# Optimization experiments

Measured on AMD Instinct MI355X. Metric: run time of the kernel, lower is better.

Reference implementation:

```python
import jax, jax.numpy as jnp
import numpy as np

D = 256
EXP = 4


def layer_norm(x, gamma, beta, eps=1e-5):
    mu = jnp.mean(x, axis=-1, keepdims=True)
    var = jnp.var(x, axis=-1, keepdims=True)
    return (x - mu) / jnp.sqrt(var + eps) * gamma + beta


def setup_inputs() -> dict:
    key = jax.random.key(0)
    ks = jax.random.split(key, 7)
    B, N = 8, 2048
    x = jax.random.normal(ks[0], (B, N, D), dtype=jnp.float32)
    w1 = jax.random.normal(ks[1], (D, EXP * D), dtype=jnp.float32) * (1.0 / np.sqrt(D))
    b1 = jnp.zeros((EXP * D,), dtype=jnp.float32)
    w2 = jax.random.normal(ks[2], (EXP * D, D), dtype=jnp.float32) * (1.0 / np.sqrt(EXP * D))
    b2 = jnp.zeros((D,), dtype=jnp.float32)
    g1 = jnp.ones((D,), dtype=jnp.float32)
    be1 = jnp.zeros((D,), dtype=jnp.float32)
    g2 = jnp.ones((D,), dtype=jnp.float32)
    be2 = jnp.zeros((D,), dtype=jnp.float32)
    return {"x": x, "w1": w1, "b1": b1, "w2": w2, "b2": b2,
            "gamma1": g1, "beta1": be1, "gamma2": g2, "beta2": be2}


def reference(x, w1, b1, w2, b2, gamma1, beta1, gamma2, beta2):
    # Sublayer 1: x + SA(LN(x)); SA uses raw QK^T softmax with Q=K=V=LN(x)
    h = layer_norm(x, gamma1, beta1)               # [B,N,D]
    scale = jnp.sqrt(jnp.float32(h.shape[-1]))
    scores = jnp.einsum('bnd,bmd->bnm', h, h) / scale  # [B,N,N]
    prob = jax.nn.softmax(scores, axis=-1)
    sa_out = jnp.einsum('bnm,bmd->bnd', prob, h)
    x = x + sa_out
    # Sublayer 2: x + FFN(LN(x))
    h2 = layer_norm(x, gamma2, beta2)
    ffn = jax.nn.relu(h2 @ w1 + b1) @ w2 + b2
    return x + ffn
```

## Files before the change

kernel.cpp:

```cpp
#include <hip/hip_runtime.h>
#include <hip/hip_bf16.h>

typedef unsigned short u16;
typedef unsigned int u32;
typedef __attribute__((ext_vector_type(8))) short short8;
typedef __attribute__((ext_vector_type(4))) float f32x4;

typedef unsigned int __attribute__((address_space(1))) as1_u32;
typedef unsigned int __attribute__((address_space(3))) as3_u32;

__device__ __forceinline__ void gload16(const void* g, void* l) {
    __builtin_amdgcn_global_load_lds((const as1_u32*)g, (as3_u32*)l, 16, 0, 0);
}

__device__ __forceinline__ u16 f2b(float f) {
    union { float f; unsigned u; } v; v.f = f;
    unsigned r = v.u + 0x7fffu + ((v.u >> 16) & 1u);
    return (u16)(r >> 16);
}

__global__ void transpose_cast(const float* __restrict__ src,
                               u16* __restrict__ dst, int R, int C) {
    __shared__ float tile[32][33];
    const int c0 = blockIdx.x * 32, r0 = blockIdx.y * 32;
    const int tx = threadIdx.x, ty = threadIdx.y;
#pragma unroll
    for (int i = ty; i < 32; i += 8)
        tile[i][tx] = src[(size_t)(r0 + i) * C + c0 + tx];
    __syncthreads();
#pragma unroll
    for (int i = ty; i < 32; i += 8)
        dst[(size_t)(c0 + i) * R + r0 + tx] = f2b(tile[tx][i]);
}

__global__ void transpose_bf16(const u16* __restrict__ src, u16* __restrict__ dst) {
    __shared__ u16 t[32][33];
    const int b = blockIdx.z;
    const int n0 = blockIdx.x * 32, d0 = blockIdx.y * 32;
    const int tx = threadIdx.x, ty = threadIdx.y;
    const u16* s = src + (size_t)b * (2048 * 256);
    u16* d = dst + (size_t)b * (2048 * 256);
#pragma unroll
    for (int i = ty; i < 32; i += 8)
        t[i][tx] = s[(size_t)(n0 + i) * 256 + d0 + tx];
    __syncthreads();
#pragma unroll
    for (int i = ty; i < 32; i += 8)
        d[(size_t)(d0 + i) * 2048 + n0 + tx] = t[tx][i];
}

__global__ __launch_bounds__(256) void ln_kernel(
    const float* __restrict__ x, const float* __restrict__ g,
    const float* __restrict__ be, u16* __restrict__ out) {
    const int lane = threadIdx.x & 63;
    const size_t row = (size_t)blockIdx.x * 4 + (threadIdx.x >> 6);
    const float4 v = *((const float4*)(x + row * 256) + lane);
    float s  = v.x + v.y + v.z + v.w;
    float s2 = v.x * v.x + v.y * v.y + v.z * v.z + v.w * v.w;
#pragma unroll
    for (int m = 1; m < 64; m <<= 1) {
        s  += __shfl_xor(s, m);
        s2 += __shfl_xor(s2, m);
    }
    const float mean = s * (1.0f / 256.0f);
    const float var  = s2 * (1.0f / 256.0f) - mean * mean;
    const float rstd = rsqrtf(var + 1e-5f);
    const float4 gv = *((const float4*)g + lane);
    const float4 bv = *((const float4*)be + lane);
    ushort4 o;
    o.x = f2b((v.x - mean) * rstd * gv.x + bv.x);
    o.y = f2b((v.y - mean) * rstd * gv.y + bv.y);
    o.z = f2b((v.z - mean) * rstd * gv.z + bv.z);
    o.w = f2b((v.w - mean) * rstd * gv.w + bv.w);
    *((ushort4*)(out + row * 256) + lane) = o;
}

#define ATTN_LDS_BYTES (2*65536 + 8*16*40*2)

__global__ __launch_bounds__(512) void attn_kernel(
    const u16* __restrict__ h, const u16* __restrict__ hT,
    const float* __restrict__ x, float* __restrict__ xmid) {
    extern __shared__ char smem[];
    const int tid  = threadIdx.x;
    const int w    = tid >> 6;
    const int lane = tid & 63;
    const int grp  = lane >> 4;
    const int l16  = lane & 15;
    const int qsub = w & 3;
    const int kh   = w >> 2;
    const int b    = blockIdx.y;
    const int q0   = blockIdx.x * 64;

    const u16* hb = h + (size_t)b * (2048 * 256);
    const char* hbB = (const char*)hb;
    const char* hTB = (const char*)(hT + (size_t)b * (2048 * 256));
    char* myPb = smem + 131072 + w * 1280;

    short8 qf[8];
    {
        const u16* qp = hb + (size_t)(q0 + qsub * 16 + l16) * 256 + grp * 8;
#pragma unroll
        for (int kk = 0; kk < 8; ++kk) qf[kk] = *(const short8*)(qp + kk * 32);
    }

    f32x4 oacc[16];
#pragma unroll
    for (int n = 0; n < 16; ++n) oacc[n] = (f32x4){0.f, 0.f, 0.f, 0.f};
    float m_run = -1e30f;
    float l_run = 0.f;

    const char* gK0 = hbB + ((size_t)(tid >> 5) << 9)
                          + (((tid & 31) ^ ((tid >> 5) & 7)) << 4);
    const char* gV0 = hTB + ((size_t)(tid >> 3) << 12)
                          + (((tid & 7) ^ ((tid >> 3) & 7)) << 4);

    {
        char* lK = smem + w * 1024;
        char* lV = smem + 32768 + w * 1024;
#pragma unroll
        for (int it = 0; it < 4; ++it) gload16(gK0 + (size_t)it * 8192, lK + it * 8192);
#pragma unroll
        for (int it = 0; it < 4; ++it) gload16(gV0 + (size_t)it * 262144, lV + it * 8192);
    }
    __syncthreads();

    for (int kt = 0; kt < 32; ++kt) {
        const int cur = kt & 1;
        if (kt < 31) {
            char* lK = smem + (cur ^ 1) * 65536 + w * 1024;
            char* lV = smem + (cur ^ 1) * 65536 + 32768 + w * 1024;
            const char* gK = gK0 + (size_t)(kt + 1) * 32768;
            const char* gV = gV0 + (size_t)(kt + 1) * 128;
#pragma unroll
            for (int it = 0; it < 4; ++it) gload16(gK + (size_t)it * 8192, lK + it * 8192);
#pragma unroll
            for (int it = 0; it < 4; ++it) gload16(gV + (size_t)it * 262144, lV + it * 8192);
        }
        const char* KBb = smem + cur * 65536;
        const char* VBb = KBb + 32768;

        f32x4 sacc[2];
#pragma unroll
        for (int j = 0; j < 2; ++j) sacc[j] = (f32x4){0.f, 0.f, 0.f, 0.f};
#pragma unroll
        for (int j = 0; j < 2; ++j) {
            const char* rb = KBb + ((kh * 32 + j * 16 + l16) << 9);
#pragma unroll
            for (int kk = 0; kk < 8; ++kk) {
                const int c = grp + 4 * kk;
                const int swz = (c & ~7) | ((c ^ l16) & 7);
                sacc[j] = __builtin_amdgcn_mfma_f32_16x16x32_bf16(
                    *(const short8*)(rb + (swz << 4)), qf[kk], sacc[j], 0, 0, 0);
            }
        }

        float p[2][4];
#pragma unroll
        for (int j = 0; j < 2; ++j)
#pragma unroll
            for (int r = 0; r < 4; ++r) p[j][r] = sacc[j][r] * 0.0625f;
        float m = p[0][0];
#pragma unroll
        for (int j = 0; j < 2; ++j)
#pragma unroll
            for (int r = 0; r < 4; ++r) m = fmaxf(m, p[j][r]);
        m = fmaxf(m, __shfl_xor(m, 16));
        m = fmaxf(m, __shfl_xor(m, 32));
        if (__any(m > m_run + 8.f)) {
            const float mnew  = fmaxf(m_run, m);
            const float alpha = __expf(m_run - mnew);
            m_run = mnew;
            l_run *= alpha;
            float ar[4];
#pragma unroll
            for (int r = 0; r < 4; ++r) ar[r] = __shfl(alpha, grp * 4 + r);
#pragma unroll
            for (int n = 0; n < 16; ++n)
#pragma unroll
                for (int r = 0; r < 4; ++r) oacc[n][r] *= ar[r];
        }
        float lt = 0.f;
#pragma unroll
        for (int j = 0; j < 2; ++j)
#pragma unroll
            for (int r = 0; r < 4; ++r) {
                p[j][r] = __expf(p[j][r] - m_run);
                lt += p[j][r];
            }
        lt += __shfl_xor(lt, 16);
        lt += __shfl_xor(lt, 32);
        l_run += lt;

#pragma unroll
        for (int j = 0; j < 2; ++j)
#pragma unroll
            for (int rp = 0; rp < 2; ++rp) {
                const u32 pk = (u32)f2b(p[j][rp * 2]) | ((u32)f2b(p[j][rp * 2 + 1]) << 16);
                *(u32*)(myPb + l16 * 80 + (j * 16 + grp * 4 + rp * 2) * 2) = pk;
            }

        {
            const short8 pa = *(const short8*)(myPb + l16 * 80 + grp * 16);
            const int cc2 = ((kh << 2) + grp) ^ (l16 & 7);
#pragma unroll
            for (int n = 0; n < 16; ++n) {
                const short8 bv =
                    *(const short8*)(VBb + ((n * 16 + l16) << 7) + (cc2 << 4));
                oacc[n] = __builtin_amdgcn_mfma_f32_16x16x32_bf16(pa, bv, oacc[n], 0, 0, 0);
            }
        }
        __syncthreads();
    }

    const int pair = w & 3;
    if (w >= 4) {
#pragma unroll
        for (int n = 0; n < 16; ++n)
            *(f32x4*)(smem + pair * 16384 + (n * 16 + l16) * 64 + grp * 16) = oacc[n];
        if (lane < 16) {
            float* mlp = (float*)(smem + 131072 + pair * 128);
            mlp[l16 * 2]     = m_run;
            mlp[l16 * 2 + 1] = l_run;
        }
    }
    __syncthreads();
    if (w < 4) {
        float c0[4], c1[4];
        {
            const float* mlp = (const float*)(smem + 131072 + w * 128);
#pragma unroll
            for (int r = 0; r < 4; ++r) {
                const float m0 = __shfl(m_run, grp * 4 + r);
                const float l0 = __shfl(l_run, grp * 4 + r);
                const float m1 = mlp[(grp * 4 + r) * 2];
                const float l1 = mlp[(grp * 4 + r) * 2 + 1];
                const float M  = fmaxf(m0, m1);
                const float a0 = __expf(m0 - M);
                const float a1 = __expf(m1 - M);
                const float inv = 1.0f / (l0 * a0 + l1 * a1);
                c0[r] = a0 * inv;
                c1[r] = a1 * inv;
            }
        }
        const float* xb = x + (size_t)b * (2048 * 256);
        float* ob = xmid + (size_t)b * (2048 * 256);
#pragma unroll
        for (int n = 0; n < 16; ++n) {
            const f32x4 o1 = *(const f32x4*)(smem + w * 16384 + (n * 16 + l16) * 64 + grp * 16);
#pragma unroll
            for (int r = 0; r < 4; ++r) {
                const int row = q0 + w * 16 + grp * 4 + r;
                const size_t idx = (size_t)row * 256 + n * 16 + l16;
                ob[idx] = xb[idx] + oacc[n][r] * c0[r] + o1[r] * c1[r];
            }
        }
    }
}

#define FFN_LDS_BYTES (2*65536 + 8*16*40*2 + 4096)

__global__ __launch_bounds__(512) void ffn_kernel(
    const u16* __restrict__ h2, const u16* __restrict__ w1t,
    const u16* __restrict__ w2t, const float* __restrict__ b1,
    const float* __restrict__ b2, float* __restrict__ xmid) {
    extern __shared__ char smem[];
    const int tid  = threadIdx.x;
    const int w    = tid >> 6;
    const int lane = tid & 63;
    const int grp  = lane >> 4;
    const int l16  = lane & 15;
    const int qsub = w & 3;
    const int hh   = w >> 2;
    const int t0   = blockIdx.x * 64;
    char* myAb = smem + 131072 + w * 1280;
    const char* b1lds = smem + 141312;

    short8 af[8];
    {
        const u16* ap = h2 + (size_t)(t0 + qsub * 16 + l16) * 256 + grp * 8;
#pragma unroll
        for (int kk = 0; kk < 8; ++kk) af[kk] = *(const short8*)(ap + kk * 32);
    }

    f32x4 oacc[16];
#pragma unroll
    for (int n = 0; n < 16; ++n) oacc[n] = (f32x4){0.f, 0.f, 0.f, 0.f};

    const char* g10 = (const char*)w1t + ((size_t)(tid >> 5) << 9)
                                       + (((tid & 31) ^ ((tid >> 5) & 7)) << 4);
    const char* g20 = (const char*)w2t + ((size_t)(tid >> 3) << 11)
                                       + (((tid & 7) ^ ((tid >> 3) & 7)) << 4);

    {
        char* l1 = smem + w * 1024;
        char* l2 = smem + 32768 + w * 1024;
#pragma unroll
        for (int it = 0; it < 4; ++it) gload16(g10 + (size_t)it * 8192, l1 + it * 8192);
#pragma unroll
        for (int it = 0; it < 4; ++it) gload16(g20 + (size_t)it * 131072, l2 + it * 8192);
        if (tid < 256)
            gload16((const char*)b1 + tid * 16, (char*)b1lds + tid * 16);
    }
    __syncthreads();

    for (int hc = 0; hc < 16; ++hc) {
        const int cur = hc & 1;
        if (hc < 15) {
            char* l1 = smem + (cur ^ 1) * 65536 + w * 1024;
            char* l2 = smem + (cur ^ 1) * 65536 + 32768 + w * 1024;
            const char* g1 = g10 + (size_t)(hc + 1) * 32768;
            const char* g2 = g20 + (size_t)(hc + 1) * 128;
#pragma unroll
            for (int it = 0; it < 4; ++it) gload16(g1 + (size_t)it * 8192, l1 + it * 8192);
#pragma unroll
            for (int it = 0; it < 4; ++it) gload16(g2 + (size_t)it * 131072, l2 + it * 8192);
        }
        const char* W1b = smem + cur * 65536;
        const char* W2b = W1b + 32768;

        f32x4 sacc[2];
#pragma unroll
        for (int j = 0; j < 2; ++j) sacc[j] = (f32x4){0.f, 0.f, 0.f, 0.f};
#pragma unroll
        for (int j = 0; j < 2; ++j) {
            const char* rb = W1b + ((hh * 32 + j * 16 + l16) << 9);
#pragma unroll
            for (int kk = 0; kk < 8; ++kk) {
                const int c = grp + 4 * kk;
                const int swz = (c & ~7) | ((c ^ l16) & 7);
                sacc[j] = __builtin_amdgcn_mfma_f32_16x16x32_bf16(
                    *(const short8*)(rb + (swz << 4)), af[kk], sacc[j], 0, 0, 0);
            }
        }

#pragma unroll
        for (int j = 0; j < 2; ++j) {
            const f32x4 bj = *(const f32x4*)(b1lds + (hc * 64 + hh * 32 + j * 16 + grp * 4) * 4);
#pragma unroll
            for (int rp = 0; rp < 2; ++rp) {
                const float v0 = fmaxf(sacc[j][rp * 2]     + bj[rp * 2],     0.f);
                const float v1 = fmaxf(sacc[j][rp * 2 + 1] + bj[rp * 2 + 1], 0.f);
                const u32 pk = (u32)f2b(v0) | ((u32)f2b(v1) << 16);
                *(u32*)(myAb + l16 * 80 + (j * 16 + grp * 4 + rp * 2) * 2) = pk;
            }
        }

        {
            const short8 pa = *(const short8*)(myAb + l16 * 80 + grp * 16);
            const int cc2 = ((hh << 2) + grp) ^ (l16 & 7);
#pragma unroll
            for (int n = 0; n < 16; ++n) {
                const short8 bv =
                    *(const short8*)(W2b + ((n * 16 + l16) << 7) + (cc2 << 4));
                oacc[n] = __builtin_amdgcn_mfma_f32_16x16x32_bf16(pa, bv, oacc[n], 0, 0, 0);
            }
        }
        __syncthreads();
    }

    const int pair = w & 3;
    if (w >= 4) {
#pragma unroll
        for (int n = 0; n < 16; ++n)
            *(f32x4*)(smem + pair * 16384 + (n * 16 + l16) * 64 + grp * 16) = oacc[n];
    }
    __syncthreads();
    if (w < 4) {
#pragma unroll
        for (int n = 0; n < 16; ++n) {
            const f32x4 o1 = *(const f32x4*)(smem + w * 16384 + (n * 16 + l16) * 64 + grp * 16);
            const float bias2 = b2[n * 16 + l16];
#pragma unroll
            for (int r = 0; r < 4; ++r) {
                const int row = t0 + w * 16 + grp * 4 + r;
                const size_t idx = (size_t)row * 256 + n * 16 + l16;
                xmid[idx] = xmid[idx] + oacc[n][r] + o1[r] + bias2;
            }
        }
    }
}

extern "C" void kernel_launch(void* const* d_in, const int* in_sizes, int n_in,
                              void* d_out, int out_size, void* d_ws, size_t ws_size,
                              hipStream_t stream) {
    (void)in_sizes; (void)n_in; (void)out_size; (void)ws_size;
    const float* x   = (const float*)d_in[0];
    const float* w1  = (const float*)d_in[1];
    const float* b1  = (const float*)d_in[2];
    const float* w2  = (const float*)d_in[3];
    const float* b2  = (const float*)d_in[4];
    const float* g1  = (const float*)d_in[5];
    const float* be1 = (const float*)d_in[6];
    const float* g2  = (const float*)d_in[7];
    const float* be2 = (const float*)d_in[8];
    float* out = (float*)d_out;

    char* ws = (char*)d_ws;
    u16* h   = (u16*)ws;
    u16* hT  = (u16*)(ws + 8388608);
    u16* w1t = (u16*)(ws + 16777216);
    u16* w2t = (u16*)(ws + 17301504);

    hipFuncSetAttribute((const void*)attn_kernel,
                        hipFuncAttributeMaxDynamicSharedMemorySize, ATTN_LDS_BYTES);
    hipFuncSetAttribute((const void*)ffn_kernel,
                        hipFuncAttributeMaxDynamicSharedMemorySize, FFN_LDS_BYTES);

    transpose_cast<<<dim3(32, 8), dim3(32, 8), 0, stream>>>(w1, w1t, 256, 1024);
    transpose_cast<<<dim3(8, 32), dim3(32, 8), 0, stream>>>(w2, w2t, 1024, 256);

    ln_kernel<<<4096, 256, 0, stream>>>(x, g1, be1, h);
    transpose_bf16<<<dim3(64, 8, 8), dim3(32, 8), 0, stream>>>(h, hT);
    attn_kernel<<<dim3(32, 8), 512, ATTN_LDS_BYTES, stream>>>(h, hT, x, out);

    ln_kernel<<<4096, 256, 0, stream>>>(out, g2, be2, h);
    ffn_kernel<<<256, 512, FFN_LDS_BYTES, stream>>>(h, w1t, w2t, b1, b2, out);
}
```

Measured before the change: 198.0 us.

## Restructure attention and FFN warp split to keep P in registers via 16x16x16 MFMA

Rebuilds the per-wave work split in both the attention and FFN kernels. Each wave now owns a quarter of the key/hidden tile and two 16-row query strips, so every K/W1 fragment loaded from LDS feeds two MFMAs. The softmax/ReLU output is passed straight from the accumulator layout into 16x16x16 bf16 MFMAs, dropping the LDS round-trip for P. The four partial results per row are merged with a 4-way split-softmax reduction through LDS, and the launch grid is remapped with batch interleaved. Register pressure rises with doubled accumulators, and the reduction epilogue needs extra LDS traffic and barriers.

```diff
diff --git a/kernel.cpp b/kernel.cpp
--- a/kernel.cpp
+++ b/kernel.cpp
@@ -4,6 +4,7 @@
 typedef unsigned short u16;
 typedef unsigned int u32;
 typedef __attribute__((ext_vector_type(8))) short short8;
+typedef __attribute__((ext_vector_type(4))) short short4v;
 typedef __attribute__((ext_vector_type(4))) float f32x4;
 
 typedef unsigned int __attribute__((address_space(1))) as1_u32;
@@ -17,6 +18,14 @@
     union { float f; unsigned u; } v; v.f = f;
     unsigned r = v.u + 0x7fffu + ((v.u >> 16) & 1u);
     return (u16)(r >> 16);
+}
+
+__device__ __forceinline__ f32x4 mfma32(short8 a, short8 b, f32x4 c) {
+    return __builtin_amdgcn_mfma_f32_16x16x32_bf16(a, b, c, 0, 0, 0);
+}
+__device__ __forceinline__ f32x4 mfma16(short4v a, short4v b, f32x4 c) {
+    asm("v_mfma_f32_16x16x16_bf16 %0, %1, %2, %0" : "+v"(c) : "v"(a), "v"(b));
+    return c;
 }
 
 __global__ void transpose_cast(const float* __restrict__ src,
@@ -75,9 +84,9 @@
     *((ushort4*)(out + row * 256) + lane) = o;
 }
 
-#define ATTN_LDS_BYTES (2*65536 + 8*16*40*2)
-
-__global__ __launch_bounds__(512) void attn_kernel(
+#define ATTN_LDS_BYTES (2*65536 + 2048)
+
+__global__ __launch_bounds__(512, 2) void attn_kernel(
     const u16* __restrict__ h, const u16* __restrict__ hT,
     const float* __restrict__ x, float* __restrict__ xmid) {
     extern __shared__ char smem[];
@@ -86,28 +95,31 @@
     const int lane = tid & 63;
     const int grp  = lane >> 4;
     const int l16  = lane & 15;
-    const int qsub = w & 3;
-    const int kh   = w >> 2;
-    const int b    = blockIdx.y;
-    const int q0   = blockIdx.x * 64;
+    const int kvq  = w & 3;
+    const int qh   = w >> 2;
+    const int bid  = blockIdx.x;
+    const int b    = bid & 7;
+    const int q0   = (bid >> 3) * 64;
 
     const u16* hb = h + (size_t)b * (2048 * 256);
     const char* hbB = (const char*)hb;
     const char* hTB = (const char*)(hT + (size_t)b * (2048 * 256));
-    char* myPb = smem + 131072 + w * 1280;
-
-    short8 qf[8];
-    {
-        const u16* qp = hb + (size_t)(q0 + qsub * 16 + l16) * 256 + grp * 8;
-#pragma unroll
-        for (int kk = 0; kk < 8; ++kk) qf[kk] = *(const short8*)(qp + kk * 32);
-    }
-
-    f32x4 oacc[16];
-#pragma unroll
-    for (int n = 0; n < 16; ++n) oacc[n] = (f32x4){0.f, 0.f, 0.f, 0.f};
-    float m_run = -1e30f;
-    float l_run = 0.f;
+
+    short8 qf[2][8];
+#pragma unroll
+    for (int st = 0; st < 2; ++st) {
+        const u16* qp = hb + (size_t)(q0 + qh * 32 + st * 16 + l16) * 256 + grp * 8;
+#pragma unroll
+        for (int kk = 0; kk < 8; ++kk) qf[st][kk] = *(const short8*)(qp + kk * 32);
+    }
+
+    f32x4 oacc[2][16];
+#pragma unroll
+    for (int st = 0; st < 2; ++st)
+#pragma unroll
+        for (int dt = 0; dt < 16; ++dt) oacc[st][dt] = (f32x4){0.f, 0.f, 0.f, 0.f};
+    float m_run[2] = {-1e30f, -1e30f};
+    float l_run[2] = {0.f, 0.f};
 
     const char* gK0 = hbB + ((size_t)(tid >> 5) << 9)
                           + (((tid & 31) ^ ((tid >> 5) & 7)) << 4);
@@ -136,130 +148,138 @@
 #pragma unroll
             for (int it = 0; it < 4; ++it) gload16(gV + (size_t)it * 262144, lV + it * 8192);
         }
-        const char* KBb = smem + cur * 65536;
-        const char* VBb = KBb + 32768;
-
-        f32x4 sacc[2];
-#pragma unroll
-        for (int j = 0; j < 2; ++j) sacc[j] = (f32x4){0.f, 0.f, 0.f, 0.f};
+        const char* KB = smem + cur * 65536;
+        const char* VB = KB + 32768;
+
+        f32x4 sacc[2] = {(f32x4){0.f,0.f,0.f,0.f}, (f32x4){0.f,0.f,0.f,0.f}};
+        const char* rb = KB + ((kvq * 16 + l16) << 9);
+#pragma unroll
+        for (int kk = 0; kk < 8; ++kk) {
+            const int c = grp + 4 * kk;
+            const int swz = (c & ~7) | ((c ^ l16) & 7);
+            const short8 kf = *(const short8*)(rb + (swz << 4));
+            sacc[0] = mfma32(kf, qf[0][kk], sacc[0]);
+            sacc[1] = mfma32(kf, qf[1][kk], sacc[1]);
+        }
+
+        short4v pa[2];
+#pragma unroll
+        for (int st = 0; st < 2; ++st) {
+            float p0 = sacc[st][0] * 0.0625f, p1 = sacc[st][1] * 0.0625f;
+            float p2 = sacc[st][2] * 0.0625f, p3 = sacc[st][3] * 0.0625f;
+            float mx = fmaxf(fmaxf(p0, p1), fmaxf(p2, p3));
+            mx = fmaxf(mx, __shfl_xor(mx, 16));
+            mx = fmaxf(mx, __shfl_xor(mx, 32));
+            if (__any(mx > m_run[st] + 8.f)) {
+                const float mnew  = fmaxf(m_run[st], mx);
+                const float alpha = __expf(m_run[st] - mnew);
+                m_run[st] = mnew;
+                l_run[st] *= alpha;
+                float ar[4];
+#pragma unroll
+                for (int r = 0; r < 4; ++r) ar[r] = __shfl(alpha, grp * 4 + r);
+#pragma unroll
+                for (int dt = 0; dt < 16; ++dt)
+#pragma unroll
+                    for (int r = 0; r < 4; ++r) oacc[st][dt][r] *= ar[r];
+            }
+            const float e0 = __expf(p0 - m_run[st]);
+            const float e1 = __expf(p1 - m_run[st]);
+            const float e2 = __expf(p2 - m_run[st]);
+            const float e3 = __expf(p3 - m_run[st]);
+            float lt = e0 + e1 + e2 + e3;
+            lt += __shfl_xor(lt, 16);
+            lt += __shfl_xor(lt, 32);
+            l_run[st] += lt;
+            pa[st] = (short4v){(short)f2b(e0), (short)f2b(e1),
+                               (short)f2b(e2), (short)f2b(e3)};
+        }
+
+        const char* vbase = VB + l16 * 128
+                          + (((kvq * 2 + (grp >> 1)) ^ (l16 & 7)) << 4)
+                          + (grp & 1) * 8;
+#pragma unroll
+        for (int dt = 0; dt < 16; ++dt) {
+            const short4v bv = *(const short4v*)(vbase + dt * 2048);
+            oacc[0][dt] = mfma16(pa[0], bv, oacc[0][dt]);
+            oacc[1][dt] = mfma16(pa[1], bv, oacc[1][dt]);
+        }
+        __syncthreads();
+    }
+
+    float2* ml = (float2*)(smem + 131072);
+    if (lane < 16) {
+        float2 t0; t0.x = m_run[0]; t0.y = l_run[0];
+        float2 t1; t1.x = m_run[1]; t1.y = l_run[1];
+        ml[w * 32 + lane]      = t0;
+        ml[w * 32 + 16 + lane] = t1;
+    }
+    const int dq = w & 3;
+    float an[2][4][4];
+    const float* xb = x + (size_t)b * (2048 * 256);
+    float* ob = xmid + (size_t)b * (2048 * 256);
+#pragma unroll
+    for (int rnd = 0; rnd < 2; ++rnd) {
+        char* wb = smem + w * 16384;
+#pragma unroll
+        for (int st = 0; st < 2; ++st)
+#pragma unroll
+            for (int k = 0; k < 8; ++k)
+                *(f32x4*)(wb + ((st * 8 + k) * 64 + lane) * 16) = oacc[st][rnd * 8 + k];
+        __syncthreads();
+        if (rnd == 0) {
+#pragma unroll
+            for (int st = 0; st < 2; ++st)
+#pragma unroll
+                for (int rr = 0; rr < 4; ++rr) {
+                    const int q = st * 16 + grp * 4 + rr;
+                    float mv[4], lv[4];
+#pragma unroll
+                    for (int kq = 0; kq < 4; ++kq) {
+                        const float2 t = ml[(qh * 4 + kq) * 32 + q];
+                        mv[kq] = t.x; lv[kq] = t.y;
+                    }
+                    const float M = fmaxf(fmaxf(mv[0], mv[1]), fmaxf(mv[2], mv[3]));
+                    float a[4], L = 0.f;
+#pragma unroll
+                    for (int kq = 0; kq < 4; ++kq) {
+                        a[kq] = __expf(mv[kq] - M);
+                        L += a[kq] * lv[kq];
+                    }
+                    const float inv = 1.0f / L;
+#pragma unroll
+                    for (int kq = 0; kq < 4; ++kq) an[st][rr][kq] = a[kq] * inv;
+                }
+        }
 #pragma unroll
         for (int j = 0; j < 2; ++j) {
-            const char* rb = KBb + ((kh * 32 + j * 16 + l16) << 9);
-#pragma unroll
-            for (int kk = 0; kk < 8; ++kk) {
-                const int c = grp + 4 * kk;
-                const int swz = (c & ~7) | ((c ^ l16) & 7);
-                sacc[j] = __builtin_amdgcn_mfma_f32_16x16x32_bf16(
-                    *(const short8*)(rb + (swz << 4)), qf[kk], sacc[j], 0, 0, 0);
+            const int dtg = rnd * 8 + dq * 2 + j;
+#pragma unroll
+            for (int st = 0; st < 2; ++st) {
+                f32x4 acc = (f32x4){0.f, 0.f, 0.f, 0.f};
+#pragma unroll
+                for (int kq = 0; kq < 4; ++kq) {
+                    const f32x4 ch = *(const f32x4*)(smem + (qh * 4 + kq) * 16384
+                                     + ((st * 8 + dq * 2 + j) * 64 + lane) * 16);
+#pragma unroll
+                    for (int rr = 0; rr < 4; ++rr) acc[rr] += an[st][rr][kq] * ch[rr];
+                }
+                const int col = dtg * 16 + l16;
+#pragma unroll
+                for (int rr = 0; rr < 4; ++rr) {
+                    const int row = q0 + qh * 32 + st * 16 + grp * 4 + rr;
+                    const size_t idx = (size_t)row * 256 + col;
+                    ob[idx] = xb[idx] + acc[rr];
+                }
             }
         }
-
-        float p[2][4];
-#pragma unroll
-        for (int j = 0; j < 2; ++j)
-#pragma unroll
-            for (int r = 0; r < 4; ++r) p[j][r] = sacc[j][r] * 0.0625f;
-        float m = p[0][0];
-#pragma unroll
-        for (int j = 0; j < 2; ++j)
-#pragma unroll
-            for (int r = 0; r < 4; ++r) m = fmaxf(m, p[j][r]);
-        m = fmaxf(m, __shfl_xor(m, 16));
-        m = fmaxf(m, __shfl_xor(m, 32));
-        if (__any(m > m_run + 8.f)) {
-            const float mnew  = fmaxf(m_run, m);
-            const float alpha = __expf(m_run - mnew);
-            m_run = mnew;
-            l_run *= alpha;
-            float ar[4];
-#pragma unroll
-            for (int r = 0; r < 4; ++r) ar[r] = __shfl(alpha, grp * 4 + r);
-#pragma unroll
-            for (int n = 0; n < 16; ++n)
-#pragma unroll
-                for (int r = 0; r < 4; ++r) oacc[n][r] *= ar[r];
-        }
-        float lt = 0.f;
-#pragma unroll
-        for (int j = 0; j < 2; ++j)
-#pragma unroll
-            for (int r = 0; r < 4; ++r) {
-                p[j][r] = __expf(p[j][r] - m_run);
-                lt += p[j][r];
-            }
-        lt += __shfl_xor(lt, 16);
-        lt += __shfl_xor(lt, 32);
-        l_run += lt;
-
-#pragma unroll
-        for (int j = 0; j < 2; ++j)
-#pragma unroll
-            for (int rp = 0; rp < 2; ++rp) {
-                const u32 pk = (u32)f2b(p[j][rp * 2]) | ((u32)f2b(p[j][rp * 2 + 1]) << 16);
-                *(u32*)(myPb + l16 * 80 + (j * 16 + grp * 4 + rp * 2) * 2) = pk;
-            }
-
-        {
-            const short8 pa = *(const short8*)(myPb + l16 * 80 + grp * 16);
-            const int cc2 = ((kh << 2) + grp) ^ (l16 & 7);
-#pragma unroll
-            for (int n = 0; n < 16; ++n) {
-                const short8 bv =
-                    *(const short8*)(VBb + ((n * 16 + l16) << 7) + (cc2 << 4));
-                oacc[n] = __builtin_amdgcn_mfma_f32_16x16x32_bf16(pa, bv, oacc[n], 0, 0, 0);
-            }
-        }
-        __syncthreads();
-    }
-
-    const int pair = w & 3;
-    if (w >= 4) {
-#pragma unroll
-        for (int n = 0; n < 16; ++n)
-            *(f32x4*)(smem + pair * 16384 + (n * 16 + l16) * 64 + grp * 16) = oacc[n];
-        if (lane < 16) {
-            float* mlp = (float*)(smem + 131072 + pair * 128);
-            mlp[l16 * 2]     = m_run;
-            mlp[l16 * 2 + 1] = l_run;
-        }
-    }
-    __syncthreads();
-    if (w < 4) {
-        float c0[4], c1[4];
-        {
-            const float* mlp = (const float*)(smem + 131072 + w * 128);
-#pragma unroll
-            for (int r = 0; r < 4; ++r) {
-                const float m0 = __shfl(m_run, grp * 4 + r);
-                const float l0 = __shfl(l_run, grp * 4 + r);
-                const float m1 = mlp[(grp * 4 + r) * 2];
-                const float l1 = mlp[(grp * 4 + r) * 2 + 1];
-                const float M  = fmaxf(m0, m1);
-                const float a0 = __expf(m0 - M);
-                const float a1 = __expf(m1 - M);
-                const float inv = 1.0f / (l0 * a0 + l1 * a1);
-                c0[r] = a0 * inv;
-                c1[r] = a1 * inv;
-            }
-        }
-        const float* xb = x + (size_t)b * (2048 * 256);
-        float* ob = xmid + (size_t)b * (2048 * 256);
-#pragma unroll
-        for (int n = 0; n < 16; ++n) {
-            const f32x4 o1 = *(const f32x4*)(smem + w * 16384 + (n * 16 + l16) * 64 + grp * 16);
-#pragma unroll
-            for (int r = 0; r < 4; ++r) {
-                const int row = q0 + w * 16 + grp * 4 + r;
-                const size_t idx = (size_t)row * 256 + n * 16 + l16;
-                ob[idx] = xb[idx] + oacc[n][r] * c0[r] + o1[r] * c1[r];
-            }
-        }
-    }
-}
-
-#define FFN_LDS_BYTES (2*65536 + 8*16*40*2 + 4096)
-
-__global__ __launch_bounds__(512) void ffn_kernel(
+        if (rnd == 0) __syncthreads();
+    }
+}
+
+#define FFN_LDS_BYTES (2*65536 + 4096)
+
+__global__ __launch_bounds__(512, 2) void ffn_kernel(
     const u16* __restrict__ h2, const u16* __restrict__ w1t,
     const u16* __restrict__ w2t, const float* __restrict__ b1,
     const float* __restrict__ b2, float* __restrict__ xmid) {
@@ -269,22 +289,24 @@
     const int lane = tid & 63;
     const int grp  = lane >> 4;
     const int l16  = lane & 15;
-    const int qsub = w & 3;
-    const int hh   = w >> 2;
+    const int hq   = w & 3;
+    const int th   = w >> 2;
     const int t0   = blockIdx.x * 64;
-    char* myAb = smem + 131072 + w * 1280;
-    const char* b1lds = smem + 141312;
-
-    short8 af[8];
-    {
-        const u16* ap = h2 + (size_t)(t0 + qsub * 16 + l16) * 256 + grp * 8;
-#pragma unroll
-        for (int kk = 0; kk < 8; ++kk) af[kk] = *(const short8*)(ap + kk * 32);
-    }
-
-    f32x4 oacc[16];
-#pragma unroll
-    for (int n = 0; n < 16; ++n) oacc[n] = (f32x4){0.f, 0.f, 0.f, 0.f};
+    char* b1lds = smem + 131072;
+
+    short8 af[2][8];
+#pragma unroll
+    for (int st = 0; st < 2; ++st) {
+        const u16* ap = h2 + (size_t)(t0 + th * 32 + st * 16 + l16) * 256 + grp * 8;
+#pragma unroll
+        for (int kk = 0; kk < 8; ++kk) af[st][kk] = *(const short8*)(ap + kk * 32);
+    }
+
+    f32x4 oacc[2][16];
+#pragma unroll
+    for (int st = 0; st < 2; ++st)
+#pragma unroll
+        for (int dt = 0; dt < 16; ++dt) oacc[st][dt] = (f32x4){0.f, 0.f, 0.f, 0.f};
 
     const char* g10 = (const char*)w1t + ((size_t)(tid >> 5) << 9)
                                        + (((tid & 31) ^ ((tid >> 5) & 7)) << 4);
@@ -298,8 +320,7 @@
         for (int it = 0; it < 4; ++it) gload16(g10 + (size_t)it * 8192, l1 + it * 8192);
 #pragma unroll
         for (int it = 0; it < 4; ++it) gload16(g20 + (size_t)it * 131072, l2 + it * 8192);
-        if (tid < 256)
-            gload16((const char*)b1 + tid * 16, (char*)b1lds + tid * 16);
+        if (tid < 256) gload16((const char*)b1 + tid * 16, b1lds + tid * 16);
     }
     __syncthreads();
 
@@ -315,68 +336,78 @@
 #pragma unroll
             for (int it = 0; it < 4; ++it) gload16(g2 + (size_t)it * 131072, l2 + it * 8192);
         }
-        const char* W1b = smem + cur * 65536;
-        const char* W2b = W1b + 32768;
-
-        f32x4 sacc[2];
-#pragma unroll
-        for (int j = 0; j < 2; ++j) sacc[j] = (f32x4){0.f, 0.f, 0.f, 0.f};
+        const char* W1B = smem + cur * 65536;
+        const char* W2B = W1B + 32768;
+
+        f32x4 sacc[2] = {(f32x4){0.f,0.f,0.f,0.f}, (f32x4){0.f,0.f,0.f,0.f}};
+        const char* rb = W1B + ((hq * 16 + l16) << 9);
+#pragma unroll
+        for (int kk = 0; kk < 8; ++kk) {
+            const int c = grp + 4 * kk;
+            const int swz = (c & ~7) | ((c ^ l16) & 7);
+            const short8 wf = *(const short8*)(rb + (swz << 4));
+            sacc[0] = mfma32(wf, af[0][kk], sacc[0]);
+            sacc[1] = mfma32(wf, af[1][kk], sacc[1]);
+        }
+
+        const f32x4 bb = *(const f32x4*)(b1lds + (hc * 64 + hq * 16 + grp * 4) * 4);
+        short4v pa[2];
+#pragma unroll
+        for (int st = 0; st < 2; ++st) {
+            const float v0 = fmaxf(sacc[st][0] + bb[0], 0.f);
+            const float v1 = fmaxf(sacc[st][1] + bb[1], 0.f);
+            const float v2 = fmaxf(sacc[st][2] + bb[2], 0.f);
+            const float v3 = fmaxf(sacc[st][3] + bb[3], 0.f);
+            pa[st] = (short4v){(short)f2b(v0), (short)f2b(v1),
+                               (short)f2b(v2), (short)f2b(v3)};
+        }
+
+        const char* vbase = W2B + l16 * 128
+                          + (((hq * 2 + (grp >> 1)) ^ (l16 & 7)) << 4)
+                          + (grp & 1) * 8;
+#pragma unroll
+        for (int dt = 0; dt < 16; ++dt) {
+            const short4v bv = *(const short4v*)(vbase + dt * 2048);
+            oacc[0][dt] = mfma16(pa[0], bv, oacc[0][dt]);
+            oacc[1][dt] = mfma16(pa[1], bv, oacc[1][dt]);
+        }
+        __syncthreads();
+    }
+
+    const int dq = w & 3;
+#pragma unroll
+    for (int rnd = 0; rnd < 2; ++rnd) {
+        char* wb = smem + w * 16384;
+#pragma unroll
+        for (int st = 0; st < 2; ++st)
+#pragma unroll
+            for (int k = 0; k < 8; ++k)
+                *(f32x4*)(wb + ((st * 8 + k) * 64 + lane) * 16) = oacc[st][rnd * 8 + k];
+        __syncthreads();
 #pragma unroll
         for (int j = 0; j < 2; ++j) {
-            const char* rb = W1b + ((hh * 32 + j * 16 + l16) << 9);
-#pragma unroll
-            for (int kk = 0; kk < 8; ++kk) {
-                const int c = grp + 4 * kk;
-                const int swz = (c & ~7) | ((c ^ l16) & 7);
-                sacc[j] = __builtin_amdgcn_mfma_f32_16x16x32_bf16(
-                    *(const short8*)(rb + (swz << 4)), af[kk], sacc[j], 0, 0, 0);
+            const int dtg = rnd * 8 + dq * 2 + j;
+            const int col = dtg * 16 + l16;
+            const float b2v = b2[col];
+#pragma unroll
+            for (int st = 0; st < 2; ++st) {
+                f32x4 acc = (f32x4){0.f, 0.f, 0.f, 0.f};
+#pragma unroll
+                for (int kq = 0; kq < 4; ++kq) {
+                    const f32x4 ch = *(const f32x4*)(smem + (th * 4 + kq) * 16384
+                                     + ((st * 8 + dq * 2 + j) * 64 + lane) * 16);
+#pragma unroll
+                    for (int rr = 0; rr < 4; ++rr) acc[rr] += ch[rr];
+                }
+#pragma unroll
+                for (int rr = 0; rr < 4; ++rr) {
+                    const int row = t0 + th * 32 + st * 16 + grp * 4 + rr;
+                    const size_t idx = (size_t)row * 256 + col;
+                    xmid[idx] = xmid[idx] + acc[rr] + b2v;
+                }
             }
         }
-
-#pragma unroll
-        for (int j = 0; j < 2; ++j) {
-            const f32x4 bj = *(const f32x4*)(b1lds + (hc * 64 + hh * 32 + j * 16 + grp * 4) * 4);
-#pragma unroll
-            for (int rp = 0; rp < 2; ++rp) {
-                const float v0 = fmaxf(sacc[j][rp * 2]     + bj[rp * 2],     0.f);
-                const float v1 = fmaxf(sacc[j][rp * 2 + 1] + bj[rp * 2 + 1], 0.f);
-                const u32 pk = (u32)f2b(v0) | ((u32)f2b(v1) << 16);
-                *(u32*)(myAb + l16 * 80 + (j * 16 + grp * 4 + rp * 2) * 2) = pk;
-            }
-        }
-
-        {
-            const short8 pa = *(const short8*)(myAb + l16 * 80 + grp * 16);
-            const int cc2 = ((hh << 2) + grp) ^ (l16 & 7);
-#pragma unroll
-            for (int n = 0; n < 16; ++n) {
-                const short8 bv =
-                    *(const short8*)(W2b + ((n * 16 + l16) << 7) + (cc2 << 4));
-                oacc[n] = __builtin_amdgcn_mfma_f32_16x16x32_bf16(pa, bv, oacc[n], 0, 0, 0);
-            }
-        }
-        __syncthreads();
-    }
-
-    const int pair = w & 3;
-    if (w >= 4) {
-#pragma unroll
-        for (int n = 0; n < 16; ++n)
-            *(f32x4*)(smem + pair * 16384 + (n * 16 + l16) * 64 + grp * 16) = oacc[n];
-    }
-    __syncthreads();
-    if (w < 4) {
-#pragma unroll
-        for (int n = 0; n < 16; ++n) {
-            const f32x4 o1 = *(const f32x4*)(smem + w * 16384 + (n * 16 + l16) * 64 + grp * 16);
-            const float bias2 = b2[n * 16 + l16];
-#pragma unroll
-            for (int r = 0; r < 4; ++r) {
-                const int row = t0 + w * 16 + grp * 4 + r;
-                const size_t idx = (size_t)row * 256 + n * 16 + l16;
-                xmid[idx] = xmid[idx] + oacc[n][r] + o1[r] + bias2;
-            }
-        }
+        if (rnd == 0) __syncthreads();
     }
 }
 
@@ -411,7 +442,7 @@
 
     ln_kernel<<<4096, 256, 0, stream>>>(x, g1, be1, h);
     transpose_bf16<<<dim3(64, 8, 8), dim3(32, 8), 0, stream>>>(h, hT);
-    attn_kernel<<<dim3(32, 8), 512, ATTN_LDS_BYTES, stream>>>(h, hT, x, out);
+    attn_kernel<<<256, 512, ATTN_LDS_BYTES, stream>>>(h, hT, x, out);
 
     ln_kernel<<<4096, 256, 0, stream>>>(out, g2, be2, h);
     ffn_kernel<<<256, 512, FFN_LDS_BYTES, stream>>>(h, w1t, w2t, b1, b2, out);
```

New measurement: 199.0 us. About the same (+0.5%).
